# Optimization experiments

Measured on AMD Instinct MI355X. Metric: run time of the kernel, lower is better.

## Reference

```python
import jax, jax.numpy as jnp
import numpy as np

B, T, N, K, DEG = 4, 256, 4096, 64, 4
L = T - 1                # number of transition steps
NNZ = B * N * DEG        # COO entries per step


def setup_inputs() -> dict:
    key = jax.random.key(0)
    k1, k2, k3, k4, k5 = jax.random.split(key, 5)
    observation = jax.random.normal(k1, (B, T, K), dtype=jnp.float32)
    W_em = jax.random.normal(k2, (K, N), dtype=jnp.float32) * 0.05
    duration = jax.random.randint(k3, (B,), 1, T + 1)  # in [1, T]
    # COO layout: for each batch b and each source state s, DEG outgoing edges
    src = jnp.tile(jnp.repeat(jnp.arange(N, dtype=jnp.int32), DEG), (B,))   # [NNZ]
    bidx = jnp.repeat(jnp.arange(B, dtype=jnp.int32), N * DEG)              # [NNZ]
    tgt = jax.random.randint(k4, (L, NNZ), 0, N, dtype=jnp.int32)
    # guarantee a self-loop so every target state has >=1 incoming edge
    self_mask = (jnp.arange(NNZ) % DEG) == 0
    tgt = jnp.where(self_mask[None, :], src[None, :], tgt)
    trans_idx = jnp.stack([jnp.broadcast_to(bidx, (L, NNZ)),
                           jnp.broadcast_to(src, (L, NNZ)),
                           tgt], axis=-1)                                   # [L,NNZ,3]
    trans_logvals = jnp.log(jax.random.uniform(k5, (L, NNZ), minval=0.1, maxval=1.0,
                                               dtype=jnp.float32))
    return {"observation": observation, "W_em": W_em, "duration": duration,
            "trans_idx": trans_idx, "trans_logvals": trans_logvals}


def _forward_alpha(observation, W_em, trans_idx, trans_logvals):
    # emission log-probs [B,T,N]
    em = jax.nn.log_softmax(jnp.einsum('btk,kn->btn', observation, W_em), axis=-1)
    la0 = em[:, 0, :] - jnp.log(jnp.float32(N))  # uniform start distribution

    def step(la_prev, inp):
        idx, lv, e = inp  # idx [NNZ,3], lv [NNZ], e [B,N]
        b, s, t = idx[:, 0], idx[:, 1], idx[:, 2]
        seg = b * N + t
        contrib = la_prev[b, s] + lv  # log_alpha[b,src] + log A[b,src,tgt]
        # numerically-stable segmented logsumexp over incoming edges per (b,tgt)
        m = jax.ops.segment_max(contrib, seg, num_segments=B * N)
        m_safe = jnp.where(jnp.isfinite(m), m, 0.0)
        ssum = jax.ops.segment_sum(jnp.exp(contrib - m_safe[seg]), seg,
                                   num_segments=B * N)
        ssum_safe = jnp.where(ssum > 0, ssum, 1.0)
        la = jnp.where(ssum > 0, jnp.log(ssum_safe) + m_safe, -jnp.inf)
        la = la.reshape(B, N) + e
        return la, la

    em_t = jnp.swapaxes(em, 0, 1)  # [T,B,N]
    _, las = jax.lax.scan(step, la0, (trans_idx, trans_logvals, em_t[1:]))
    log_alpha = jnp.concatenate([la0[None], las], axis=0)  # [T,B,N]
    return jnp.swapaxes(log_alpha, 0, 1)  # [B,T,N]


def reference(observation, W_em, duration, trans_idx, trans_logvals):
    log_alpha = _forward_alpha(observation, W_em, trans_idx, trans_logvals)
    log_sums = jax.nn.logsumexp(log_alpha, axis=2)                # [B,T]
    log_probs = jnp.take_along_axis(log_sums, duration[:, None] - 1, axis=1)  # [B,1]
    return log_probs
```

## Files before the change

kernel.cpp:

```cpp
#include <hip/hip_runtime.h>
#include <hip/hip_bf16.h>

#define Bc 4
#define Tc 256
#define Nc 4096
#define Kc 64
#define DEGc 4
#define Lc (Tc - 1)
#define NNZc (Bc * Nc * DEGc)
#define NPB 16
#define TPB 256
#define NODES_PER (Nc / NPB)
#define EDGES_PER ((Nc * DEGc) / NPB)
#define LOG_N 8.31776616671934f

__device__ __forceinline__ float cohLoadF(float* p) {
  return __hip_atomic_load(p, __ATOMIC_RELAXED, __HIP_MEMORY_SCOPE_AGENT);
}
__device__ __forceinline__ void cohStoreF(float* p, float v) {
  __hip_atomic_store(p, v, __ATOMIC_RELAXED, __HIP_MEMORY_SCOPE_AGENT);
}

__device__ __forceinline__ float blockSum(float v, volatile float* red) {
#pragma unroll
  for (int o = 1; o < 64; o <<= 1) v += __shfl_xor(v, o, 64);
  __syncthreads();
  if ((threadIdx.x & 63) == 0) red[threadIdx.x >> 6] = v;
  __syncthreads();
  return red[0] + red[1] + red[2] + red[3];
}
__device__ __forceinline__ float blockMax(float v, volatile float* red) {
#pragma unroll
  for (int o = 1; o < 64; o <<= 1) v = fmaxf(v, __shfl_xor(v, o, 64));
  __syncthreads();
  if ((threadIdx.x & 63) == 0) red[threadIdx.x >> 6] = v;
  __syncthreads();
  return fmaxf(fmaxf(red[0], red[1]), fmaxf(red[2], red[3]));
}

__global__ __launch_bounds__(TPB) void em_kernel(const float* __restrict__ obs,
                                                 const float* __restrict__ W,
                                                 float* __restrict__ em) {
  const int r = blockIdx.x, tid = threadIdx.x;
  __shared__ float o[Kc];
  __shared__ float red[8];
  if (tid < Kc) o[tid] = obs[(size_t)r * Kc + tid];
  __syncthreads();
  float4 acc[4];
#pragma unroll
  for (int gI = 0; gI < 4; ++gI) acc[gI] = make_float4(0.f, 0.f, 0.f, 0.f);
  const float4* W4 = (const float4*)W;
  for (int k = 0; k < Kc; ++k) {
    const float ov = o[k];
    const float4* wr = W4 + (size_t)k * (Nc / 4);
#pragma unroll
    for (int gI = 0; gI < 4; ++gI) {
      float4 w = wr[gI * 256 + tid];
      acc[gI].x = fmaf(ov, w.x, acc[gI].x);
      acc[gI].y = fmaf(ov, w.y, acc[gI].y);
      acc[gI].z = fmaf(ov, w.z, acc[gI].z);
      acc[gI].w = fmaf(ov, w.w, acc[gI].w);
    }
  }
  float m = -INFINITY;
#pragma unroll
  for (int gI = 0; gI < 4; ++gI)
    m = fmaxf(m, fmaxf(fmaxf(acc[gI].x, acc[gI].y), fmaxf(acc[gI].z, acc[gI].w)));
  m = blockMax(m, red);
  float s = 0.f;
#pragma unroll
  for (int gI = 0; gI < 4; ++gI)
    s += __expf(acc[gI].x - m) + __expf(acc[gI].y - m) + __expf(acc[gI].z - m) + __expf(acc[gI].w - m);
  s = blockSum(s, red);
  const float lse = m + __logf(s);
  float4* em4 = (float4*)em;
#pragma unroll
  for (int gI = 0; gI < 4; ++gI) {
    float4 w = acc[gI];
    w.x -= lse; w.y -= lse; w.z -= lse; w.w -= lse;
    em4[(size_t)r * (Nc / 4) + gI * 256 + tid] = w;
  }
}

__global__ __launch_bounds__(TPB) void scan_kernel(
    const int* __restrict__ duration,
    const int* __restrict__ tidx,
    const float* __restrict__ tlv,
    const float* __restrict__ em,
    float* __restrict__ sbuf,
    float* __restrict__ S,
    unsigned int* __restrict__ cnt,
    float* __restrict__ out) {
  const int g = blockIdx.x;
  const int b = g / NPB, sl = g % NPB;
  const int tid = threadIdx.x;
  __shared__ float red[8];

  const int node = sl * NODES_PER + tid;
  const int ebase = b * (Nc * DEGc) + sl * EDGES_PER + tid * 4;
  unsigned int* mycnt = cnt + b * 16;

  float la = em[((size_t)b * Tc) * Nc + node] - LOG_N;
  {
    float tot = blockSum(__expf(la), red);
    if (tid == 0) unsafeAtomicAdd(&S[0 * Bc + b], tot);
  }

  int4 c0, c1, c2; float4 cl;
  {
    const size_t e = (size_t)ebase;
    const int4* ip = (const int4*)tidx + ((e * 3) >> 2);
    c0 = ip[0]; c1 = ip[1]; c2 = ip[2];
    cl = ((const float4*)tlv)[e >> 2];
  }

  for (int t = 1; t <= Lc; ++t) {
    int4 n0 = c0, n1 = c1, n2 = c2; float4 nl = cl;
    if (t < Lc) {
      const size_t e = (size_t)t * NNZc + (size_t)ebase;
      const int4* ip = (const int4*)tidx + ((e * 3) >> 2);
      n0 = ip[0]; n1 = ip[1]; n2 = ip[2];
      nl = ((const float4*)tlv)[e >> 2];
    }
    const float em_t = em[((size_t)b * Tc + t) * Nc + node];

    float* sb = sbuf + (size_t)(t & 1) * (Bc * Nc) + (size_t)b * Nc;
    unsafeAtomicAdd(&sb[c0.z], __expf(la + cl.x));
    unsafeAtomicAdd(&sb[c1.y], __expf(la + cl.y));
    unsafeAtomicAdd(&sb[c2.x], __expf(la + cl.z));
    unsafeAtomicAdd(&sb[c2.w], __expf(la + cl.w));

    __syncthreads();
    if (tid == 0) {
      __builtin_amdgcn_sched_barrier(0);
      __hip_atomic_fetch_add(mycnt, 1u, __ATOMIC_RELAXED, __HIP_MEMORY_SCOPE_AGENT);
      const unsigned target = (unsigned)NPB * (unsigned)t;
      while (__hip_atomic_load(mycnt, __ATOMIC_RELAXED, __HIP_MEMORY_SCOPE_AGENT) < target)
        __builtin_amdgcn_s_sleep(1);
      __builtin_amdgcn_sched_barrier(0);
    }
    __syncthreads();

    float sv = cohLoadF(&sb[node]);
    cohStoreF(&sb[node], 0.0f);
    const float logSp = __logf(cohLoadF(&S[(t - 1) * Bc + b]));
    const float v = __logf(sv) + em_t;
    float tot = blockSum(__expf(v), red);
    if (tid == 0) unsafeAtomicAdd(&S[t * Bc + b], tot);
    la = v - logSp;

    c0 = n0; c1 = n1; c2 = n2; cl = nl;
  }

  __syncthreads();
  if (tid == 0) {
    __builtin_amdgcn_sched_barrier(0);
    __hip_atomic_fetch_add(mycnt, 1u, __ATOMIC_RELAXED, __HIP_MEMORY_SCOPE_AGENT);
    const unsigned target = (unsigned)NPB * (unsigned)Tc;
    while (__hip_atomic_load(mycnt, __ATOMIC_RELAXED, __HIP_MEMORY_SCOPE_AGENT) < target)
      __builtin_amdgcn_s_sleep(1);
    __builtin_amdgcn_sched_barrier(0);
  }
  __syncthreads();

  if (sl == 0) {
    const int tstar = duration[b] - 1;
    const int tau = tid;
    float v = 0.0f;
    if (tau == tstar || tau <= tstar - 2)
      v = __logf(cohLoadF(&S[tau * Bc + b]));
    float tot = blockSum(v, red);
    if (tid == 0) out[b] = tot;
  }
}

extern "C" void kernel_launch(void* const* d_in, const int* in_sizes, int n_in,
                              void* d_out, int out_size, void* d_ws, size_t ws_size,
                              hipStream_t stream) {
  const float* obs = (const float*)d_in[0];
  const float* W = (const float*)d_in[1];
  const int* duration = (const int*)d_in[2];
  const int* tidx = (const int*)d_in[3];
  const float* tlv = (const float*)d_in[4];
  float* out = (float*)d_out;

  float* em = (float*)d_ws;
  float* sbuf = em + (size_t)Bc * Tc * Nc;
  float* S = sbuf + (size_t)2 * Bc * Nc;
  unsigned int* cnt = (unsigned int*)(S + (size_t)Tc * Bc);

  const size_t zero_bytes =
      ((size_t)2 * Bc * Nc + (size_t)Tc * Bc) * sizeof(float) + 64 * sizeof(unsigned int);
  hipMemsetAsync(sbuf, 0, zero_bytes, stream);

  em_kernel<<<dim3(Bc * Tc), dim3(TPB), 0, stream>>>(obs, W, em);
  scan_kernel<<<dim3(Bc * NPB), dim3(TPB), 0, stream>>>(duration, tidx, tlv, em,
                                                        sbuf, S, cnt, out);
}
```

Baseline: 1.521 ms.

## Scatter into shared-memory partials per block instead of global float atomics

Each block now accumulates its scattered exp contributions into a full-size LDS buffer with shared atomics. It then writes a per-block partial vector to global memory, and each node sums the NPB partials after the grid barrier. This replaces contended global atomicAdds and the per-step global zeroing. Blocks per batch drop from 16 to 8 with 512 threads, and tidx/tlv/em loads are prefetched two steps ahead. The trade is more global write and read traffic per step (NPB×N floats per batch) and per-step LDS zeroing.

```diff
diff --git a/kernel.cpp b/kernel.cpp
--- a/kernel.cpp
+++ b/kernel.cpp
@@ -1,5 +1,6 @@
 #include <hip/hip_runtime.h>
 #include <hip/hip_bf16.h>
+
 
 #define Bc 4
 #define Tc 256
@@ -8,39 +9,47 @@
 #define DEGc 4
 #define Lc (Tc - 1)
 #define NNZc (Bc * Nc * DEGc)
-#define NPB 16
-#define TPB 256
+#define NPB 8
+#define TPB 512
+#define TPB_EM 256
 #define NODES_PER (Nc / NPB)
-#define EDGES_PER ((Nc * DEGc) / NPB)
 #define LOG_N 8.31776616671934f
 
-__device__ __forceinline__ float cohLoadF(float* p) {
-  return __hip_atomic_load(p, __ATOMIC_RELAXED, __HIP_MEMORY_SCOPE_AGENT);
+__device__ __forceinline__ float cohLoadF(const float* p) {
+  return __hip_atomic_load((float*)p, __ATOMIC_RELAXED, __HIP_MEMORY_SCOPE_AGENT);
 }
 __device__ __forceinline__ void cohStoreF(float* p, float v) {
   __hip_atomic_store(p, v, __ATOMIC_RELAXED, __HIP_MEMORY_SCOPE_AGENT);
 }
 
-__device__ __forceinline__ float blockSum(float v, volatile float* red) {
+template <int NT>
+__device__ __forceinline__ float blockSumT(float v, volatile float* red) {
 #pragma unroll
   for (int o = 1; o < 64; o <<= 1) v += __shfl_xor(v, o, 64);
   __syncthreads();
   if ((threadIdx.x & 63) == 0) red[threadIdx.x >> 6] = v;
   __syncthreads();
-  return red[0] + red[1] + red[2] + red[3];
-}
-__device__ __forceinline__ float blockMax(float v, volatile float* red) {
+  float s = 0.f;
+#pragma unroll
+  for (int k = 0; k < NT / 64; ++k) s += red[k];
+  return s;
+}
+template <int NT>
+__device__ __forceinline__ float blockMaxT(float v, volatile float* red) {
 #pragma unroll
   for (int o = 1; o < 64; o <<= 1) v = fmaxf(v, __shfl_xor(v, o, 64));
   __syncthreads();
   if ((threadIdx.x & 63) == 0) red[threadIdx.x >> 6] = v;
   __syncthreads();
-  return fmaxf(fmaxf(red[0], red[1]), fmaxf(red[2], red[3]));
-}
-
-__global__ __launch_bounds__(TPB) void em_kernel(const float* __restrict__ obs,
-                                                 const float* __restrict__ W,
-                                                 float* __restrict__ em) {
+  float m = -INFINITY;
+#pragma unroll
+  for (int k = 0; k < NT / 64; ++k) m = fmaxf(m, red[k]);
+  return m;
+}
+
+__global__ __launch_bounds__(TPB_EM) void em_kernel(const float* __restrict__ obs,
+                                                    const float* __restrict__ W,
+                                                    float* __restrict__ em) {
   const int r = blockIdx.x, tid = threadIdx.x;
   __shared__ float o[Kc];
   __shared__ float red[8];
@@ -66,12 +75,12 @@
 #pragma unroll
   for (int gI = 0; gI < 4; ++gI)
     m = fmaxf(m, fmaxf(fmaxf(acc[gI].x, acc[gI].y), fmaxf(acc[gI].z, acc[gI].w)));
-  m = blockMax(m, red);
+  m = blockMaxT<TPB_EM>(m, red);
   float s = 0.f;
 #pragma unroll
   for (int gI = 0; gI < 4; ++gI)
     s += __expf(acc[gI].x - m) + __expf(acc[gI].y - m) + __expf(acc[gI].z - m) + __expf(acc[gI].w - m);
-  s = blockSum(s, red);
+  s = blockSumT<TPB_EM>(s, red);
   const float lse = m + __logf(s);
   float4* em4 = (float4*)em;
 #pragma unroll
@@ -87,89 +96,122 @@
     const int* __restrict__ tidx,
     const float* __restrict__ tlv,
     const float* __restrict__ em,
-    float* __restrict__ sbuf,
-    float* __restrict__ S,
+    float* __restrict__ part,
+    float* __restrict__ Spart,
     unsigned int* __restrict__ cnt,
     float* __restrict__ out) {
   const int g = blockIdx.x;
   const int b = g / NPB, sl = g % NPB;
   const int tid = threadIdx.x;
-  __shared__ float red[8];
+  __shared__ float red[TPB / 64];
+  __shared__ float lsb[Nc];
 
   const int node = sl * NODES_PER + tid;
-  const int ebase = b * (Nc * DEGc) + sl * EDGES_PER + tid * 4;
+  const size_t ebase = (size_t)b * (Nc * DEGc) + (size_t)node * DEGc;
   unsigned int* mycnt = cnt + b * 16;
 
+#pragma unroll
+  for (int i = 0; i < Nc / TPB; ++i) lsb[i * TPB + tid] = 0.f;
+
   float la = em[((size_t)b * Tc) * Nc + node] - LOG_N;
-  {
-    float tot = blockSum(__expf(la), red);
-    if (tid == 0) unsafeAtomicAdd(&S[0 * Bc + b], tot);
-  }
-
   int4 c0, c1, c2; float4 cl;
   {
-    const size_t e = (size_t)ebase;
+    const int4* ip = (const int4*)tidx + ((ebase * 3) >> 2);
+    c0 = ip[0]; c1 = ip[1]; c2 = ip[2];
+    cl = ((const float4*)tlv)[ebase >> 2];
+  }
+  int4 n0, n1, n2; float4 nl;
+  {
+    const size_t e = ebase + (size_t)NNZc;
     const int4* ip = (const int4*)tidx + ((e * 3) >> 2);
-    c0 = ip[0]; c1 = ip[1]; c2 = ip[2];
-    cl = ((const float4*)tlv)[e >> 2];
+    n0 = ip[0]; n1 = ip[1]; n2 = ip[2];
+    nl = ((const float4*)tlv)[e >> 2];
+  }
+  float em_nxt = em[((size_t)b * Tc + 1) * Nc + node];
+
+  {
+    float tot = blockSumT<TPB>(__expf(la), red);
+    if (tid == 0) cohStoreF(&Spart[(0 * Bc + b) * 16 + sl], tot);
   }
 
   for (int t = 1; t <= Lc; ++t) {
-    int4 n0 = c0, n1 = c1, n2 = c2; float4 nl = cl;
-    if (t < Lc) {
-      const size_t e = (size_t)t * NNZc + (size_t)ebase;
-      const int4* ip = (const int4*)tidx + ((e * 3) >> 2);
-      n0 = ip[0]; n1 = ip[1]; n2 = ip[2];
-      nl = ((const float4*)tlv)[e >> 2];
-    }
-    const float em_t = em[((size_t)b * Tc + t) * Nc + node];
-
-    float* sb = sbuf + (size_t)(t & 1) * (Bc * Nc) + (size_t)b * Nc;
-    unsafeAtomicAdd(&sb[c0.z], __expf(la + cl.x));
-    unsafeAtomicAdd(&sb[c1.y], __expf(la + cl.y));
-    unsafeAtomicAdd(&sb[c2.x], __expf(la + cl.z));
-    unsafeAtomicAdd(&sb[c2.w], __expf(la + cl.w));
-
+    atomicAdd(&lsb[c0.z], __expf(la + cl.x));
+    atomicAdd(&lsb[c1.y], __expf(la + cl.y));
+    atomicAdd(&lsb[c2.x], __expf(la + cl.z));
+    atomicAdd(&lsb[c2.w], __expf(la + cl.w));
     __syncthreads();
+
+    float* pp = part + (((size_t)(t & 1) * Bc + b) * NPB + sl) * Nc;
+#pragma unroll
+    for (int i = 0; i < Nc / TPB; ++i) {
+      const int j = i * TPB + tid;
+      float pv = lsb[j];
+      lsb[j] = 0.f;
+      cohStoreF(&pp[j], pv);
+    }
+    __syncthreads();
+
     if (tid == 0) {
-      __builtin_amdgcn_sched_barrier(0);
       __hip_atomic_fetch_add(mycnt, 1u, __ATOMIC_RELAXED, __HIP_MEMORY_SCOPE_AGENT);
       const unsigned target = (unsigned)NPB * (unsigned)t;
       while (__hip_atomic_load(mycnt, __ATOMIC_RELAXED, __HIP_MEMORY_SCOPE_AGENT) < target)
         __builtin_amdgcn_s_sleep(1);
-      __builtin_amdgcn_sched_barrier(0);
     }
     __syncthreads();
 
-    float sv = cohLoadF(&sb[node]);
-    cohStoreF(&sb[node], 0.0f);
-    const float logSp = __logf(cohLoadF(&S[(t - 1) * Bc + b]));
-    const float v = __logf(sv) + em_t;
-    float tot = blockSum(__expf(v), red);
-    if (tid == 0) unsafeAtomicAdd(&S[t * Bc + b], tot);
-    la = v - logSp;
+    const float* pbase = part + ((size_t)(t & 1) * Bc + b) * NPB * Nc;
+    float pk[NPB];
+#pragma unroll
+    for (int k = 0; k < NPB; ++k) pk[k] = cohLoadF(&pbase[(size_t)k * Nc + node]);
+    float Sprev = 0.f;
+#pragma unroll
+    for (int k = 0; k < NPB; ++k) Sprev += cohLoadF(&Spart[((size_t)(t - 1) * Bc + b) * 16 + k]);
+
+    int4 m0 = n0, m1 = n1, m2 = n2; float4 ml = nl;
+    if (t <= Lc - 2) {
+      const size_t e = (size_t)(t + 1) * NNZc + ebase;
+      const int4* ip = (const int4*)tidx + ((e * 3) >> 2);
+      m0 = ip[0]; m1 = ip[1]; m2 = ip[2];
+      ml = ((const float4*)tlv)[e >> 2];
+    }
+    float em_fut = em_nxt;
+    if (t < Lc) em_fut = em[((size_t)b * Tc + t + 1) * Nc + node];
+
+    float sv = 0.f;
+#pragma unroll
+    for (int k = 0; k < NPB; ++k) sv += pk[k];
+    const float v = __logf(sv) + em_nxt;
+    float tot = blockSumT<TPB>(__expf(v), red);
+    if (tid == 0) cohStoreF(&Spart[((size_t)t * Bc + b) * 16 + sl], tot);
+    la = v - __logf(Sprev);
 
     c0 = n0; c1 = n1; c2 = n2; cl = nl;
+    n0 = m0; n1 = m1; n2 = m2; nl = ml;
+    em_nxt = em_fut;
   }
 
   __syncthreads();
   if (tid == 0) {
-    __builtin_amdgcn_sched_barrier(0);
     __hip_atomic_fetch_add(mycnt, 1u, __ATOMIC_RELAXED, __HIP_MEMORY_SCOPE_AGENT);
     const unsigned target = (unsigned)NPB * (unsigned)Tc;
     while (__hip_atomic_load(mycnt, __ATOMIC_RELAXED, __HIP_MEMORY_SCOPE_AGENT) < target)
       __builtin_amdgcn_s_sleep(1);
-    __builtin_amdgcn_sched_barrier(0);
   }
   __syncthreads();
 
   if (sl == 0) {
     const int tstar = duration[b] - 1;
-    const int tau = tid;
     float v = 0.0f;
-    if (tau == tstar || tau <= tstar - 2)
-      v = __logf(cohLoadF(&S[tau * Bc + b]));
-    float tot = blockSum(v, red);
+    if (tid < Tc) {
+      const int tau = tid;
+      if (tau == tstar || tau <= tstar - 2) {
+        float Sv = 0.f;
+#pragma unroll
+        for (int k = 0; k < NPB; ++k) Sv += cohLoadF(&Spart[((size_t)tau * Bc + b) * 16 + k]);
+        v = __logf(Sv);
+      }
+    }
+    float tot = blockSumT<TPB>(v, red);
     if (tid == 0) out[b] = tot;
   }
 }
@@ -185,15 +227,13 @@
   float* out = (float*)d_out;
 
   float* em = (float*)d_ws;
-  float* sbuf = em + (size_t)Bc * Tc * Nc;
-  float* S = sbuf + (size_t)2 * Bc * Nc;
-  unsigned int* cnt = (unsigned int*)(S + (size_t)Tc * Bc);
-
-  const size_t zero_bytes =
-      ((size_t)2 * Bc * Nc + (size_t)Tc * Bc) * sizeof(float) + 64 * sizeof(unsigned int);
-  hipMemsetAsync(sbuf, 0, zero_bytes, stream);
-
-  em_kernel<<<dim3(Bc * Tc), dim3(TPB), 0, stream>>>(obs, W, em);
+  float* part = em + (size_t)Bc * Tc * Nc;
+  float* Spart = part + (size_t)2 * Bc * NPB * Nc;
+  unsigned int* cnt = (unsigned int*)(Spart + (size_t)Tc * Bc * 16);
+
+  hipMemsetAsync(cnt, 0, 64 * sizeof(unsigned int), stream);
+
+  em_kernel<<<dim3(Bc * Tc), dim3(TPB_EM), 0, stream>>>(obs, W, em);
   scan_kernel<<<dim3(Bc * NPB), dim3(TPB), 0, stream>>>(duration, tidx, tlv, em,
-                                                        sbuf, S, cnt, out);
-}
+                                                        part, Spart, cnt, out);
+}
```

Result: slower. 1.733 ms (+14.0%).
